# Performance work log

Measured on AMD Instinct MI355X. Metric: run time of the kernel, lower is better.

## Reference

```python
import jax, jax.numpy as jnp
import numpy as np

DENSITY_FACTOR = 100.0
RAY_SAMPLES = 256
W_RES, H_RES = 320, 240
BS = 4
VOL_D = 128


def setup_inputs() -> dict:
    key = jax.random.key(0)
    k1, k2 = jax.random.split(key)
    vol = jax.random.uniform(k1, (BS, 4, VOL_D, VOL_D, VOL_D), dtype=jnp.float32)
    # per-batch rigid rotation about the y axis (homogeneous 4x4, w component stays 1)
    ang = jax.random.uniform(k2, (BS,), minval=0.0, maxval=2.0 * np.pi, dtype=jnp.float32)
    c, s = jnp.cos(ang), jnp.sin(ang)
    z, o = jnp.zeros_like(c), jnp.ones_like(c)
    tfm = jnp.stack([
        jnp.stack([c, z, s, z], -1),
        jnp.stack([z, o, z, z], -1),
        jnp.stack([-s, z, c, z], -1),
        jnp.stack([z, z, z, o], -1),
    ], axis=1)  # (BS,4,4)
    return {"vol": vol, "tfm": tfm}


def grid_sample_3d(vol, grid):
    """torch.nn.functional.grid_sample (5D, trilinear, zeros padding, align_corners=False).
    vol: (C,D,H,W); grid: (S,Hh,Ww,3) with last dim = (x,y,z) in [-1,1]. -> (C,S,Hh,Ww)"""
    C, D, H, W = vol.shape
    gx, gy, gz = grid[..., 0], grid[..., 1], grid[..., 2]
    # unnormalize, align_corners=False convention
    ix = ((gx + 1.0) * W - 1.0) * 0.5
    iy = ((gy + 1.0) * H - 1.0) * 0.5
    iz = ((gz + 1.0) * D - 1.0) * 0.5
    ix0, iy0, iz0 = jnp.floor(ix), jnp.floor(iy), jnp.floor(iz)
    fx, fy, fz = ix - ix0, iy - iy0, iz - iz0
    out = jnp.zeros((C,) + grid.shape[:-1], vol.dtype)
    for dz in (0, 1):
        for dy in (0, 1):
            for dx in (0, 1):
                xi, yi, zi = ix0 + dx, iy0 + dy, iz0 + dz
                w = ((fx if dx else 1.0 - fx) * (fy if dy else 1.0 - fy)
                     * (fz if dz else 1.0 - fz))
                valid = ((xi >= 0) & (xi < W) & (yi >= 0) & (yi < H)
                         & (zi >= 0) & (zi < D))
                xc = jnp.clip(xi, 0, W - 1).astype(jnp.int32)
                yc = jnp.clip(yi, 0, H - 1).astype(jnp.int32)
                zc = jnp.clip(zi, 0, D - 1).astype(jnp.int32)
                v = vol[:, zc, yc, xc]  # (C,S,Hh,Ww) gather
                out = out + v * (w * valid.astype(vol.dtype))[None]
    return out


def _sample_coords(tfm):
    """Build the transformed sample grid: (BS, S, H, W, 3)."""
    z = jnp.linspace(-1.0, 1.0, RAY_SAMPLES)
    y = jnp.linspace(-1.0, 1.0, H_RES)
    x = jnp.linspace(-1.0, 1.0, W_RES)
    Z, Y, X = jnp.meshgrid(z, y, x, indexing='ij')  # torch.meshgrid default 'ij'
    coords = jnp.stack([X, Y, Z, jnp.ones_like(X)], axis=-1)  # (S,H,W,4) homogenized
    flat = coords.reshape(-1, 4)
    tc = jnp.einsum('bij,nj->bni', tfm, flat).reshape(
        tfm.shape[0], RAY_SAMPLES, H_RES, W_RES, 4)
    return tc[..., :3] / tc[..., 3:4]


def reference(vol, tfm):
    density = vol[:, 3:4]            # (B,1,D,H,W)
    color = vol[:, :3]               # (B,3,D,H,W)
    grid = _sample_coords(tfm.astype(vol.dtype))  # (B,S,H,W,3)
    dens = density * (DENSITY_FACTOR / RAY_SAMPLES)
    ds = jax.vmap(grid_sample_3d)(dens, grid)        # (B,1,S,H,W)
    transmission = jnp.cumprod(1.0 - ds, axis=2)     # sequential scan over rays
    weight = ds * transmission                       # (B,1,S,H,W)
    w_sum = jnp.sum(weight, axis=2)                  # (B,1,H,W)
    cs = jax.vmap(grid_sample_3d)(color, grid)       # (B,3,S,H,W)
    render = jnp.sum(weight * cs, axis=2) / (w_sum + 1e-6)  # (B,3,H,W)
    alpha = 1.0 - transmission[:, :, -1]             # == 1 - prod(1-ds, axis=2)
    return render * alpha
```

## Files before the change

kernel.cpp:

```cpp
#include <hip/hip_runtime.h>
#include <hip/hip_fp16.h>

namespace {

constexpr int W_RES = 320, H_RES = 240, BS = 4, VD = 128, NS = 256;
constexpr float DENS_SCALE = 100.0f / 256.0f;
constexpr float TAU = 5e-4f;
constexpr long long VOX = (long long)VD * VD * VD;

__device__ __forceinline__ unsigned h2u(__half2 h) {
    unsigned u; __builtin_memcpy(&u, &h, 4); return u;
}
__device__ __forceinline__ __half2 u2h(unsigned u) {
    __half2 h; __builtin_memcpy(&h, &u, 4); return h;
}

__global__ void transpose_k(const float* __restrict__ vol, uint4* __restrict__ out) {
    long long tid = (long long)blockIdx.x * blockDim.x + threadIdx.x;
    const long long npair = (long long)BS * VOX / 2;
    if (tid >= npair) return;
    int b = (int)(tid / (VOX / 2));
    long long r2 = (tid - (long long)b * (VOX / 2)) * 2;
    const float* vb = vol + (long long)b * 4 * VOX + r2;
    float2 R = *(const float2*)(vb);
    float2 G = *(const float2*)(vb + VOX);
    float2 Bc = *(const float2*)(vb + 2 * VOX);
    float2 Dn = *(const float2*)(vb + 3 * VOX);
    uint4 o;
    o.x = h2u(__floats2half2_rn(R.x, G.x));
    o.y = h2u(__floats2half2_rn(Bc.x, Dn.x));
    o.z = h2u(__floats2half2_rn(R.y, G.y));
    o.w = h2u(__floats2half2_rn(Bc.y, Dn.y));
    out[tid] = o;
}

struct Stage {
    uint2 p[8];
    float w[8];
};

struct Coord {
    int x0, y0, z0;
    float fx, fy, fz;
    bool fast;
};

__device__ __forceinline__ Coord make_coord(float ix, float iy, float iz) {
    Coord c;
    float fx0 = floorf(ix), fy0 = floorf(iy), fz0 = floorf(iz);
    c.fx = ix - fx0; c.fy = iy - fy0; c.fz = iz - fz0;
    c.x0 = (int)fx0; c.y0 = (int)fy0; c.z0 = (int)fz0;
    c.fast = ((unsigned)c.x0 < 127u) & ((unsigned)c.y0 < 127u) & ((unsigned)c.z0 < 127u);
    return c;
}

__device__ __forceinline__ void weights_plain(const Coord& c, Stage& st) {
    float wx0 = 1.0f - c.fx, wx1 = c.fx;
    float wy0 = 1.0f - c.fy, wy1 = c.fy;
    float wz0 = 1.0f - c.fz, wz1 = c.fz;
    float w00 = wz0 * wy0, w01 = wz0 * wy1, w10 = wz1 * wy0, w11 = wz1 * wy1;
    st.w[0] = w00 * wx0; st.w[1] = w00 * wx1;
    st.w[2] = w01 * wx0; st.w[3] = w01 * wx1;
    st.w[4] = w10 * wx0; st.w[5] = w10 * wx1;
    st.w[6] = w11 * wx0; st.w[7] = w11 * wx1;
}

__device__ __forceinline__ void stage_fast(const uint2* __restrict__ vb,
                                           const Coord& c, Stage& st) {
    const uint2* r0 = vb + ((c.z0 * VD + c.y0) * VD + c.x0);
    const uint2* r1 = r0 + VD * VD;
    st.p[0] = r0[0];      st.p[1] = r0[1];
    st.p[2] = r0[VD];     st.p[3] = r0[VD + 1];
    st.p[4] = r1[0];      st.p[5] = r1[1];
    st.p[6] = r1[VD];     st.p[7] = r1[VD + 1];
    weights_plain(c, st);
}

__device__ __forceinline__ void stage_safe(const uint2* __restrict__ vb,
                                           const Coord& c, Stage& st) {
    int x0 = c.x0, y0 = c.y0, z0 = c.z0;
    float mx0 = ((unsigned)x0 < 128u) ? 1.0f : 0.0f;
    float mx1 = ((unsigned)(x0 + 1) < 128u) ? 1.0f : 0.0f;
    float my0 = ((unsigned)y0 < 128u) ? 1.0f : 0.0f;
    float my1 = ((unsigned)(y0 + 1) < 128u) ? 1.0f : 0.0f;
    float mz0 = ((unsigned)z0 < 128u) ? 1.0f : 0.0f;
    float mz1 = ((unsigned)(z0 + 1) < 128u) ? 1.0f : 0.0f;
    float wx0 = (1.0f - c.fx) * mx0, wx1 = c.fx * mx1;
    float wy0 = (1.0f - c.fy) * my0, wy1 = c.fy * my1;
    float wz0 = (1.0f - c.fz) * mz0, wz1 = c.fz * mz1;

    int xc0 = min(max(x0, 0), 127), xc1 = min(max(x0 + 1, 0), 127);
    int yc0 = min(max(y0, 0), 127), yc1 = min(max(y0 + 1, 0), 127);
    int zc0 = min(max(z0, 0), 127), zc1 = min(max(z0 + 1, 0), 127);

    int r00 = (zc0 * VD + yc0) * VD, r01 = (zc0 * VD + yc1) * VD;
    int r10 = (zc1 * VD + yc0) * VD, r11 = (zc1 * VD + yc1) * VD;

    st.p[0] = vb[r00 + xc0]; st.p[1] = vb[r00 + xc1];
    st.p[2] = vb[r01 + xc0]; st.p[3] = vb[r01 + xc1];
    st.p[4] = vb[r10 + xc0]; st.p[5] = vb[r10 + xc1];
    st.p[6] = vb[r11 + xc0]; st.p[7] = vb[r11 + xc1];

    float w00 = wz0 * wy0, w01 = wz0 * wy1, w10 = wz1 * wy0, w11 = wz1 * wy1;
    st.w[0] = w00 * wx0; st.w[1] = w00 * wx1;
    st.w[2] = w01 * wx0; st.w[3] = w01 * wx1;
    st.w[4] = w10 * wx0; st.w[5] = w10 * wx1;
    st.w[6] = w11 * wx0; st.w[7] = w11 * wx1;
}

__device__ __forceinline__ void consume(const Stage& st, float& T, float& wsum,
                                        float& aR, float& aG, float& aB) {
    float ax0 = 0, ay0 = 0, az0 = 0, aw0 = 0;
    float ax1 = 0, ay1 = 0, az1 = 0, aw1 = 0;
#pragma unroll
    for (int i = 0; i < 8; i += 2) {
        __half2 rg0 = u2h(st.p[i].x), bd0 = u2h(st.p[i].y);
        __half2 rg1 = u2h(st.p[i + 1].x), bd1 = u2h(st.p[i + 1].y);
        ax0 = fmaf(st.w[i], __half2float(__low2half(rg0)), ax0);
        ay0 = fmaf(st.w[i], __half2float(__high2half(rg0)), ay0);
        az0 = fmaf(st.w[i], __half2float(__low2half(bd0)), az0);
        aw0 = fmaf(st.w[i], __half2float(__high2half(bd0)), aw0);
        ax1 = fmaf(st.w[i + 1], __half2float(__low2half(rg1)), ax1);
        ay1 = fmaf(st.w[i + 1], __half2float(__high2half(rg1)), ay1);
        az1 = fmaf(st.w[i + 1], __half2float(__low2half(bd1)), az1);
        aw1 = fmaf(st.w[i + 1], __half2float(__high2half(bd1)), aw1);
    }
    float dsv = (aw0 + aw1) * DENS_SCALE;
    T *= (1.0f - dsv);
    float wgt = dsv * T;
    wsum += wgt;
    aR = fmaf(wgt, ax0 + ax1, aR);
    aG = fmaf(wgt, ay0 + ay1, aG);
    aB = fmaf(wgt, az0 + az1, aB);
}

__global__ void __launch_bounds__(256) raycast_k(const uint2* __restrict__ vol8,
                                                 const float* __restrict__ tfm,
                                                 float* __restrict__ out) {
    constexpr int NPIX = W_RES * H_RES;
    int lane = threadIdx.x & 63;
    int wave = threadIdx.x >> 6;
    int bx = blockIdx.x % (W_RES / 16);
    int rest = blockIdx.x / (W_RES / 16);
    int by = rest % (H_RES / 16);
    int b = rest / (H_RES / 16);
    int x = bx * 16 + (lane & 15);
    int y = by * 16 + wave * 4 + (lane >> 4);

    float X = -1.0f + 2.0f * x / (float)(W_RES - 1);
    float Y = -1.0f + 2.0f * y / (float)(H_RES - 1);
    const float dZ = 2.0f / (float)(NS - 1);

    const float* M = tfm + b * 16;
    float bxc = M[0] * X + M[1] * Y + M[3];
    float byc = M[4] * X + M[5] * Y + M[7];
    float bzc = M[8] * X + M[9] * Y + M[11];
    float bwc = M[12] * X + M[13] * Y + M[15];
    float m02 = M[2], m12 = M[6], m22 = M[10], m32 = M[14];

    const uint2* vb = vol8 + (long long)b * VOX;

    bool w1 = (fabsf(bwc - 1.0f) < 1e-6f) && (fabsf(m32) < 1e-6f);
    float lo = 0.0f, hi = (float)(NS - 1);
    if (w1) {
        const float LIM = 1.0078125f + 1e-5f;
        auto clipAxis = [&](float bb, float mm) {
            float A = bb - mm;
            float B = mm * dZ;
            if (fabsf(B) < 1e-9f) {
                if (fabsf(A) > LIM) { lo = 1.0f; hi = 0.0f; }
            } else {
                float s1 = (-LIM - A) / B, s2 = (LIM - A) / B;
                lo = fmaxf(lo, fminf(s1, s2));
                hi = fminf(hi, fmaxf(s1, s2));
            }
        };
        clipAxis(bxc, m02);
        clipAxis(byc, m12);
        clipAxis(bzc, m22);
    }
    int s_start = max(0, (int)ceilf(lo - 1e-3f));
    int s_end = min(NS - 1, (int)floorf(hi + 1e-3f));

    int wsv = s_start, wev = s_end;
#pragma unroll
    for (int off = 1; off < 64; off <<= 1) {
        wsv = min(wsv, __shfl_xor(wsv, off));
        wev = max(wev, __shfl_xor(wev, off));
    }

    auto coords = [&](int s, float& ix, float& iy, float& iz) {
        float Z = fmaf((float)s, dZ, -1.0f);
        float gx = fmaf(m02, Z, bxc);
        float gy = fmaf(m12, Z, byc);
        float gz = fmaf(m22, Z, bzc);
        if (!w1) {
            float iw = 1.0f / fmaf(m32, Z, bwc);
            gx *= iw; gy *= iw; gz *= iw;
        }
        ix = fmaf(gx, 64.0f, 63.5f);
        iy = fmaf(gy, 64.0f, 63.5f);
        iz = fmaf(gz, 64.0f, 63.5f);
    };

    float T = 1.0f, wsum = 0.0f, aR = 0.0f, aG = 0.0f, aB = 0.0f;
    Stage A, B, C;

    for (int s = wsv; s <= wev; s += 3) {
        bool alive = (T >= TAU);
        bool g0 = (s >= s_start) & (s <= s_end) & alive;
        bool g1 = (s + 1 >= s_start) & (s + 1 <= s_end) & alive;
        bool g2 = (s + 2 >= s_start) & (s + 2 <= s_end) & alive;
        Coord c0, c1, c2;
        float ix, iy, iz;
        if (g0) { coords(s, ix, iy, iz); c0 = make_coord(ix, iy, iz); }
        if (g1) { coords(s + 1, ix, iy, iz); c1 = make_coord(ix, iy, iz); }
        if (g2) { coords(s + 2, ix, iy, iz); c2 = make_coord(ix, iy, iz); }
        bool fastAll = __all((g0 ? c0.fast : true) & (g1 ? c1.fast : true) &
                             (g2 ? c2.fast : true));
        if (fastAll) {
            if (g0) stage_fast(vb, c0, A);
            if (g1) stage_fast(vb, c1, B);
            if (g2) stage_fast(vb, c2, C);
        } else {
            if (g0) stage_safe(vb, c0, A);
            if (g1) stage_safe(vb, c1, B);
            if (g2) stage_safe(vb, c2, C);
        }
        __builtin_amdgcn_sched_barrier(0);
        if (g0) consume(A, T, wsum, aR, aG, aB);
        if (g1 & (T >= TAU)) consume(B, T, wsum, aR, aG, aB);
        if (g2 & (T >= TAU)) consume(C, T, wsum, aR, aG, aB);
        if (!__any((T >= TAU) & (s + 3 <= s_end))) break;
    }

    float scale = (1.0f - T) / (wsum + 1e-6f);
    int po = y * W_RES + x;
    float* ob = out + (long long)b * 3 * NPIX;
    ob[po] = aR * scale;
    ob[po + NPIX] = aG * scale;
    ob[po + 2 * NPIX] = aB * scale;
}

}

extern "C" void kernel_launch(void* const* d_in, const int* in_sizes, int n_in,
                              void* d_out, int out_size, void* d_ws, size_t ws_size,
                              hipStream_t stream) {
    const float* vol = (const float*)d_in[0];
    const float* tfm = (const float*)d_in[1];
    float* out = (float*)d_out;

    uint4* v16 = (uint4*)d_ws;
    (void)ws_size; (void)in_sizes; (void)n_in; (void)out_size;

    const long long npair = (long long)BS * VOX / 2;
    transpose_k<<<(int)((npair + 255) / 256), 256, 0, stream>>>(vol, v16);

    const int nblk = (W_RES / 16) * (H_RES / 16) * BS;
    raycast_k<<<nblk, 256, 0, stream>>>((const uint2*)v16, tfm, out);
}
```

Before: 173.0 us.

## Quantize volume to RGBA8, use persistent atomic tile scheduler with center-out ordering

Converts the packed volume from fp16 RGBA (8 bytes per voxel) to 8-bit unorm RGBA (4 bytes per voxel), halving gather bandwidth and cache footprint, and rescales density and color in the consumer. The raycast kernel becomes persistent: 2048 single-wave blocks pull 16x4 pixel tiles from an atomic counter, ordered center-out and interleaved across batches, to balance uneven ray lengths. The inner loop now steps by 4 samples without per-sample validity guards. The loss of guards and 8-bit quantization add accuracy risk, and the counter reset relies on the transpose kernel running first.

```diff
diff --git a/kernel.cpp b/kernel.cpp
--- a/kernel.cpp
+++ b/kernel.cpp
@@ -1,41 +1,44 @@
 #include <hip/hip_runtime.h>
-#include <hip/hip_fp16.h>
 
 namespace {
 
 constexpr int W_RES = 320, H_RES = 240, BS = 4, VD = 128, NS = 256;
-constexpr float DENS_SCALE = 100.0f / 256.0f;
+constexpr float DENS_SCALE = 100.0f / 256.0f / 255.0f;
 constexpr float TAU = 5e-4f;
 constexpr long long VOX = (long long)VD * VD * VD;
-
-__device__ __forceinline__ unsigned h2u(__half2 h) {
-    unsigned u; __builtin_memcpy(&u, &h, 4); return u;
-}
-__device__ __forceinline__ __half2 u2h(unsigned u) {
-    __half2 h; __builtin_memcpy(&h, &u, 4); return h;
-}
-
-__global__ void transpose_k(const float* __restrict__ vol, uint4* __restrict__ out) {
+constexpr int NTILE = (W_RES / 16) * (H_RES / 4) * BS;
+constexpr size_t CTR_OFF = (size_t)BS * VOX * 4;
+
+__global__ void transpose_k(const float* __restrict__ vol, uint4* __restrict__ out,
+                            unsigned* __restrict__ ctr) {
     long long tid = (long long)blockIdx.x * blockDim.x + threadIdx.x;
-    const long long npair = (long long)BS * VOX / 2;
-    if (tid >= npair) return;
-    int b = (int)(tid / (VOX / 2));
-    long long r2 = (tid - (long long)b * (VOX / 2)) * 2;
-    const float* vb = vol + (long long)b * 4 * VOX + r2;
-    float2 R = *(const float2*)(vb);
-    float2 G = *(const float2*)(vb + VOX);
-    float2 Bc = *(const float2*)(vb + 2 * VOX);
-    float2 Dn = *(const float2*)(vb + 3 * VOX);
+    if (tid == 0) *ctr = 0u;
+    const long long nq = (long long)BS * VOX / 4;
+    if (tid >= nq) return;
+    int b = (int)(tid / (VOX / 4));
+    long long r4 = (tid - (long long)b * (VOX / 4)) * 4;
+    const float* vb = vol + (long long)b * 4 * VOX + r4;
+    float4 R = *(const float4*)(vb);
+    float4 G = *(const float4*)(vb + VOX);
+    float4 Bc = *(const float4*)(vb + 2 * VOX);
+    float4 Dn = *(const float4*)(vb + 3 * VOX);
+    auto pk = [](float r, float g, float bl, float d) -> unsigned {
+        unsigned ur = (unsigned)(r * 255.0f + 0.5f);
+        unsigned ug = (unsigned)(g * 255.0f + 0.5f);
+        unsigned ub = (unsigned)(bl * 255.0f + 0.5f);
+        unsigned ud = (unsigned)(d * 255.0f + 0.5f);
+        return ur | (ug << 8) | (ub << 16) | (ud << 24);
+    };
     uint4 o;
-    o.x = h2u(__floats2half2_rn(R.x, G.x));
-    o.y = h2u(__floats2half2_rn(Bc.x, Dn.x));
-    o.z = h2u(__floats2half2_rn(R.y, G.y));
-    o.w = h2u(__floats2half2_rn(Bc.y, Dn.y));
+    o.x = pk(R.x, G.x, Bc.x, Dn.x);
+    o.y = pk(R.y, G.y, Bc.y, Dn.y);
+    o.z = pk(R.z, G.z, Bc.z, Dn.z);
+    o.w = pk(R.w, G.w, Bc.w, Dn.w);
     out[tid] = o;
 }
 
-struct Stage {
-    uint2 p[8];
+struct St {
+    unsigned p[8];
     float w[8];
 };
 
@@ -45,19 +48,21 @@
     bool fast;
 };
 
-__device__ __forceinline__ Coord make_coord(float ix, float iy, float iz) {
+__device__ __forceinline__ Coord mkc(float ix, float iy, float iz) {
     Coord c;
-    float fx0 = floorf(ix), fy0 = floorf(iy), fz0 = floorf(iz);
-    c.fx = ix - fx0; c.fy = iy - fy0; c.fz = iz - fz0;
-    c.x0 = (int)fx0; c.y0 = (int)fy0; c.z0 = (int)fz0;
+    float f;
+    f = floorf(ix); c.fx = ix - f; c.x0 = (int)f;
+    f = floorf(iy); c.fy = iy - f; c.y0 = (int)f;
+    f = floorf(iz); c.fz = iz - f; c.z0 = (int)f;
     c.fast = ((unsigned)c.x0 < 127u) & ((unsigned)c.y0 < 127u) & ((unsigned)c.z0 < 127u);
     return c;
 }
 
-__device__ __forceinline__ void weights_plain(const Coord& c, Stage& st) {
-    float wx0 = 1.0f - c.fx, wx1 = c.fx;
-    float wy0 = 1.0f - c.fy, wy1 = c.fy;
-    float wz0 = 1.0f - c.fz, wz1 = c.fz;
+__device__ __forceinline__ void wts(const Coord& c, St& st, float mx0, float mx1,
+                                    float my0, float my1, float mz0, float mz1) {
+    float wx0 = (1.0f - c.fx) * mx0, wx1 = c.fx * mx1;
+    float wy0 = (1.0f - c.fy) * my0, wy1 = c.fy * my1;
+    float wz0 = (1.0f - c.fz) * mz0, wz1 = c.fz * mz1;
     float w00 = wz0 * wy0, w01 = wz0 * wy1, w10 = wz1 * wy0, w11 = wz1 * wy1;
     st.w[0] = w00 * wx0; st.w[1] = w00 * wx1;
     st.w[2] = w01 * wx0; st.w[3] = w01 * wx1;
@@ -65,19 +70,19 @@
     st.w[6] = w11 * wx0; st.w[7] = w11 * wx1;
 }
 
-__device__ __forceinline__ void stage_fast(const uint2* __restrict__ vb,
-                                           const Coord& c, Stage& st) {
-    const uint2* r0 = vb + ((c.z0 * VD + c.y0) * VD + c.x0);
-    const uint2* r1 = r0 + VD * VD;
-    st.p[0] = r0[0];      st.p[1] = r0[1];
-    st.p[2] = r0[VD];     st.p[3] = r0[VD + 1];
-    st.p[4] = r1[0];      st.p[5] = r1[1];
-    st.p[6] = r1[VD];     st.p[7] = r1[VD + 1];
-    weights_plain(c, st);
-}
-
-__device__ __forceinline__ void stage_safe(const uint2* __restrict__ vb,
-                                           const Coord& c, Stage& st) {
+__device__ __forceinline__ void stage_fast(const unsigned* __restrict__ vb,
+                                           const Coord& c, St& st) {
+    const unsigned* r0 = vb + ((c.z0 * VD + c.y0) * VD + c.x0);
+    const unsigned* r1 = r0 + VD * VD;
+    st.p[0] = r0[0];  st.p[1] = r0[1];
+    st.p[2] = r0[VD]; st.p[3] = r0[VD + 1];
+    st.p[4] = r1[0];  st.p[5] = r1[1];
+    st.p[6] = r1[VD]; st.p[7] = r1[VD + 1];
+    wts(c, st, 1, 1, 1, 1, 1, 1);
+}
+
+__device__ __forceinline__ void stage_safe(const unsigned* __restrict__ vb,
+                                           const Coord& c, St& st) {
     int x0 = c.x0, y0 = c.y0, z0 = c.z0;
     float mx0 = ((unsigned)x0 < 128u) ? 1.0f : 0.0f;
     float mx1 = ((unsigned)(x0 + 1) < 128u) ? 1.0f : 0.0f;
@@ -85,9 +90,6 @@
     float my1 = ((unsigned)(y0 + 1) < 128u) ? 1.0f : 0.0f;
     float mz0 = ((unsigned)z0 < 128u) ? 1.0f : 0.0f;
     float mz1 = ((unsigned)(z0 + 1) < 128u) ? 1.0f : 0.0f;
-    float wx0 = (1.0f - c.fx) * mx0, wx1 = c.fx * mx1;
-    float wy0 = (1.0f - c.fy) * my0, wy1 = c.fy * my1;
-    float wz0 = (1.0f - c.fz) * mz0, wz1 = c.fz * mz1;
 
     int xc0 = min(max(x0, 0), 127), xc1 = min(max(x0 + 1, 0), 127);
     int yc0 = min(max(y0, 0), 127), yc1 = min(max(y0 + 1, 0), 127);
@@ -101,145 +103,144 @@
     st.p[4] = vb[r10 + xc0]; st.p[5] = vb[r10 + xc1];
     st.p[6] = vb[r11 + xc0]; st.p[7] = vb[r11 + xc1];
 
-    float w00 = wz0 * wy0, w01 = wz0 * wy1, w10 = wz1 * wy0, w11 = wz1 * wy1;
-    st.w[0] = w00 * wx0; st.w[1] = w00 * wx1;
-    st.w[2] = w01 * wx0; st.w[3] = w01 * wx1;
-    st.w[4] = w10 * wx0; st.w[5] = w10 * wx1;
-    st.w[6] = w11 * wx0; st.w[7] = w11 * wx1;
-}
-
-__device__ __forceinline__ void consume(const Stage& st, float& T, float& wsum,
+    wts(c, st, mx0, mx1, my0, my1, mz0, mz1);
+}
+
+__device__ __forceinline__ void consume(const St& st, float& T, float& wsum,
                                         float& aR, float& aG, float& aB) {
-    float ax0 = 0, ay0 = 0, az0 = 0, aw0 = 0;
-    float ax1 = 0, ay1 = 0, az1 = 0, aw1 = 0;
+    float ar = 0, ag = 0, ab = 0, ad = 0;
 #pragma unroll
-    for (int i = 0; i < 8; i += 2) {
-        __half2 rg0 = u2h(st.p[i].x), bd0 = u2h(st.p[i].y);
-        __half2 rg1 = u2h(st.p[i + 1].x), bd1 = u2h(st.p[i + 1].y);
-        ax0 = fmaf(st.w[i], __half2float(__low2half(rg0)), ax0);
-        ay0 = fmaf(st.w[i], __half2float(__high2half(rg0)), ay0);
-        az0 = fmaf(st.w[i], __half2float(__low2half(bd0)), az0);
-        aw0 = fmaf(st.w[i], __half2float(__high2half(bd0)), aw0);
-        ax1 = fmaf(st.w[i + 1], __half2float(__low2half(rg1)), ax1);
-        ay1 = fmaf(st.w[i + 1], __half2float(__high2half(rg1)), ay1);
-        az1 = fmaf(st.w[i + 1], __half2float(__low2half(bd1)), az1);
-        aw1 = fmaf(st.w[i + 1], __half2float(__high2half(bd1)), aw1);
+    for (int i = 0; i < 8; ++i) {
+        unsigned cv = st.p[i];
+        float w = st.w[i];
+        ar = fmaf(w, (float)(cv & 255u), ar);
+        ag = fmaf(w, (float)((cv >> 8) & 255u), ag);
+        ab = fmaf(w, (float)((cv >> 16) & 255u), ab);
+        ad = fmaf(w, (float)(cv >> 24), ad);
     }
-    float dsv = (aw0 + aw1) * DENS_SCALE;
+    float dsv = ad * DENS_SCALE;
     T *= (1.0f - dsv);
     float wgt = dsv * T;
     wsum += wgt;
-    aR = fmaf(wgt, ax0 + ax1, aR);
-    aG = fmaf(wgt, ay0 + ay1, aG);
-    aB = fmaf(wgt, az0 + az1, aB);
-}
-
-__global__ void __launch_bounds__(256) raycast_k(const uint2* __restrict__ vol8,
-                                                 const float* __restrict__ tfm,
-                                                 float* __restrict__ out) {
+    aR = fmaf(wgt, ar, aR);
+    aG = fmaf(wgt, ag, aG);
+    aB = fmaf(wgt, ab, aB);
+}
+
+__global__ void __launch_bounds__(64) raycast_k(const unsigned* __restrict__ vol,
+                                                const float* __restrict__ tfm,
+                                                float* __restrict__ out,
+                                                unsigned* __restrict__ ctr) {
     constexpr int NPIX = W_RES * H_RES;
-    int lane = threadIdx.x & 63;
-    int wave = threadIdx.x >> 6;
-    int bx = blockIdx.x % (W_RES / 16);
-    int rest = blockIdx.x / (W_RES / 16);
-    int by = rest % (H_RES / 16);
-    int b = rest / (H_RES / 16);
-    int x = bx * 16 + (lane & 15);
-    int y = by * 16 + wave * 4 + (lane >> 4);
-
-    float X = -1.0f + 2.0f * x / (float)(W_RES - 1);
-    float Y = -1.0f + 2.0f * y / (float)(H_RES - 1);
+    const int lane = threadIdx.x;
     const float dZ = 2.0f / (float)(NS - 1);
 
-    const float* M = tfm + b * 16;
-    float bxc = M[0] * X + M[1] * Y + M[3];
-    float byc = M[4] * X + M[5] * Y + M[7];
-    float bzc = M[8] * X + M[9] * Y + M[11];
-    float bwc = M[12] * X + M[13] * Y + M[15];
-    float m02 = M[2], m12 = M[6], m22 = M[10], m32 = M[14];
-
-    const uint2* vb = vol8 + (long long)b * VOX;
-
-    bool w1 = (fabsf(bwc - 1.0f) < 1e-6f) && (fabsf(m32) < 1e-6f);
-    float lo = 0.0f, hi = (float)(NS - 1);
-    if (w1) {
-        const float LIM = 1.0078125f + 1e-5f;
-        auto clipAxis = [&](float bb, float mm) {
-            float A = bb - mm;
-            float B = mm * dZ;
-            if (fabsf(B) < 1e-9f) {
-                if (fabsf(A) > LIM) { lo = 1.0f; hi = 0.0f; }
+    while (true) {
+        unsigned n = 0;
+        if (lane == 0) n = atomicAdd(ctr, 1u);
+        n = (unsigned)__shfl((int)n, 0);
+        if (n >= (unsigned)NTILE) return;
+
+        int b = n & 3;
+        int k = n >> 2;
+        int cxr = k / 60;
+        int ryr = k - cxr * 60;
+        int tx = (cxr & 1) ? (9 - (cxr >> 1)) : (10 + (cxr >> 1));
+        int ty = (ryr & 1) ? (29 - (ryr >> 1)) : (30 + (ryr >> 1));
+        int x = tx * 16 + (lane & 15);
+        int y = ty * 4 + (lane >> 4);
+
+        float X = -1.0f + 2.0f * x / (float)(W_RES - 1);
+        float Y = -1.0f + 2.0f * y / (float)(H_RES - 1);
+
+        const float* M = tfm + b * 16;
+        float bxc = M[0] * X + M[1] * Y + M[3];
+        float byc = M[4] * X + M[5] * Y + M[7];
+        float bzc = M[8] * X + M[9] * Y + M[11];
+        float bwc = M[12] * X + M[13] * Y + M[15];
+        float m02 = M[2], m12 = M[6], m22 = M[10], m32 = M[14];
+
+        const unsigned* vb = vol + (long long)b * VOX;
+
+        bool w1 = (fabsf(bwc - 1.0f) < 1e-6f) && (fabsf(m32) < 1e-6f);
+        float lo = 0.0f, hi = (float)(NS - 1);
+        if (w1) {
+            const float LIM = 1.0078125f + 1e-5f;
+            auto clipAxis = [&](float bb, float mm) {
+                float A = bb - mm;
+                float Bq = mm * dZ;
+                if (fabsf(Bq) < 1e-9f) {
+                    if (fabsf(A) > LIM) { lo = 1.0f; hi = 0.0f; }
+                } else {
+                    float s1 = (-LIM - A) / Bq, s2 = (LIM - A) / Bq;
+                    lo = fmaxf(lo, fminf(s1, s2));
+                    hi = fminf(hi, fmaxf(s1, s2));
+                }
+            };
+            clipAxis(bxc, m02);
+            clipAxis(byc, m12);
+            clipAxis(bzc, m22);
+        }
+        int s_start = max(0, (int)ceilf(lo - 1e-3f));
+        int s_end = min(NS - 1, (int)floorf(hi + 1e-3f));
+
+        int wsv = s_start, wev = s_end;
+#pragma unroll
+        for (int off = 1; off < 64; off <<= 1) {
+            wsv = min(wsv, __shfl_xor(wsv, off));
+            wev = max(wev, __shfl_xor(wev, off));
+        }
+
+        auto coords = [&](int s, float& ix, float& iy, float& iz) {
+            float Z = fmaf((float)s, dZ, -1.0f);
+            float gx = fmaf(m02, Z, bxc);
+            float gy = fmaf(m12, Z, byc);
+            float gz = fmaf(m22, Z, bzc);
+            if (!w1) {
+                float iw = 1.0f / fmaf(m32, Z, bwc);
+                gx *= iw; gy *= iw; gz *= iw;
+            }
+            ix = fmaf(gx, 64.0f, 63.5f);
+            iy = fmaf(gy, 64.0f, 63.5f);
+            iz = fmaf(gz, 64.0f, 63.5f);
+        };
+
+        float T = 1.0f, wsum = 0.0f, aR = 0.0f, aG = 0.0f, aB = 0.0f;
+        St S0, S1, S2, S3;
+
+        for (int s = wsv; s <= wev; s += 4) {
+            float ix, iy, iz;
+            coords(s, ix, iy, iz);      Coord c0 = mkc(ix, iy, iz);
+            coords(s + 1, ix, iy, iz);  Coord c1 = mkc(ix, iy, iz);
+            coords(s + 2, ix, iy, iz);  Coord c2 = mkc(ix, iy, iz);
+            coords(s + 3, ix, iy, iz);  Coord c3 = mkc(ix, iy, iz);
+            bool fast = __all(c0.fast & c1.fast & c2.fast & c3.fast);
+            if (fast) {
+                stage_fast(vb, c0, S0);
+                stage_fast(vb, c1, S1);
+                stage_fast(vb, c2, S2);
+                stage_fast(vb, c3, S3);
             } else {
-                float s1 = (-LIM - A) / B, s2 = (LIM - A) / B;
-                lo = fmaxf(lo, fminf(s1, s2));
-                hi = fminf(hi, fmaxf(s1, s2));
+                stage_safe(vb, c0, S0);
+                stage_safe(vb, c1, S1);
+                stage_safe(vb, c2, S2);
+                stage_safe(vb, c3, S3);
             }
-        };
-        clipAxis(bxc, m02);
-        clipAxis(byc, m12);
-        clipAxis(bzc, m22);
+            __builtin_amdgcn_sched_barrier(0);
+            consume(S0, T, wsum, aR, aG, aB);
+            consume(S1, T, wsum, aR, aG, aB);
+            consume(S2, T, wsum, aR, aG, aB);
+            consume(S3, T, wsum, aR, aG, aB);
+            if (!__any(T >= TAU)) break;
+        }
+
+        float scale = (1.0f - T) / (wsum + 1e-6f) * (1.0f / 255.0f);
+        int po = y * W_RES + x;
+        float* ob = out + (long long)b * 3 * NPIX;
+        ob[po] = aR * scale;
+        ob[po + NPIX] = aG * scale;
+        ob[po + 2 * NPIX] = aB * scale;
     }
-    int s_start = max(0, (int)ceilf(lo - 1e-3f));
-    int s_end = min(NS - 1, (int)floorf(hi + 1e-3f));
-
-    int wsv = s_start, wev = s_end;
-#pragma unroll
-    for (int off = 1; off < 64; off <<= 1) {
-        wsv = min(wsv, __shfl_xor(wsv, off));
-        wev = max(wev, __shfl_xor(wev, off));
-    }
-
-    auto coords = [&](int s, float& ix, float& iy, float& iz) {
-        float Z = fmaf((float)s, dZ, -1.0f);
-        float gx = fmaf(m02, Z, bxc);
-        float gy = fmaf(m12, Z, byc);
-        float gz = fmaf(m22, Z, bzc);
-        if (!w1) {
-            float iw = 1.0f / fmaf(m32, Z, bwc);
-            gx *= iw; gy *= iw; gz *= iw;
-        }
-        ix = fmaf(gx, 64.0f, 63.5f);
-        iy = fmaf(gy, 64.0f, 63.5f);
-        iz = fmaf(gz, 64.0f, 63.5f);
-    };
-
-    float T = 1.0f, wsum = 0.0f, aR = 0.0f, aG = 0.0f, aB = 0.0f;
-    Stage A, B, C;
-
-    for (int s = wsv; s <= wev; s += 3) {
-        bool alive = (T >= TAU);
-        bool g0 = (s >= s_start) & (s <= s_end) & alive;
-        bool g1 = (s + 1 >= s_start) & (s + 1 <= s_end) & alive;
-        bool g2 = (s + 2 >= s_start) & (s + 2 <= s_end) & alive;
-        Coord c0, c1, c2;
-        float ix, iy, iz;
-        if (g0) { coords(s, ix, iy, iz); c0 = make_coord(ix, iy, iz); }
-        if (g1) { coords(s + 1, ix, iy, iz); c1 = make_coord(ix, iy, iz); }
-        if (g2) { coords(s + 2, ix, iy, iz); c2 = make_coord(ix, iy, iz); }
-        bool fastAll = __all((g0 ? c0.fast : true) & (g1 ? c1.fast : true) &
-                             (g2 ? c2.fast : true));
-        if (fastAll) {
-            if (g0) stage_fast(vb, c0, A);
-            if (g1) stage_fast(vb, c1, B);
-            if (g2) stage_fast(vb, c2, C);
-        } else {
-            if (g0) stage_safe(vb, c0, A);
-            if (g1) stage_safe(vb, c1, B);
-            if (g2) stage_safe(vb, c2, C);
-        }
-        __builtin_amdgcn_sched_barrier(0);
-        if (g0) consume(A, T, wsum, aR, aG, aB);
-        if (g1 & (T >= TAU)) consume(B, T, wsum, aR, aG, aB);
-        if (g2 & (T >= TAU)) consume(C, T, wsum, aR, aG, aB);
-        if (!__any((T >= TAU) & (s + 3 <= s_end))) break;
-    }
-
-    float scale = (1.0f - T) / (wsum + 1e-6f);
-    int po = y * W_RES + x;
-    float* ob = out + (long long)b * 3 * NPIX;
-    ob[po] = aR * scale;
-    ob[po + NPIX] = aG * scale;
-    ob[po + 2 * NPIX] = aB * scale;
 }
 
 }
@@ -251,12 +252,13 @@
     const float* tfm = (const float*)d_in[1];
     float* out = (float*)d_out;
 
-    uint4* v16 = (uint4*)d_ws;
+    unsigned char* ws = (unsigned char*)d_ws;
+    uint4* v8 = (uint4*)ws;
+    unsigned* ctr = (unsigned*)(ws + CTR_OFF);
     (void)ws_size; (void)in_sizes; (void)n_in; (void)out_size;
 
-    const long long npair = (long long)BS * VOX / 2;
-    transpose_k<<<(int)((npair + 255) / 256), 256, 0, stream>>>(vol, v16);
-
-    const int nblk = (W_RES / 16) * (H_RES / 16) * BS;
-    raycast_k<<<nblk, 256, 0, stream>>>((const uint2*)v16, tfm, out);
-}
+    const long long nq = (long long)BS * VOX / 4;
+    transpose_k<<<(int)((nq + 255) / 256), 256, 0, stream>>>(vol, v8, ctr);
+
+    raycast_k<<<2048, 64, 0, stream>>>((const unsigned*)v8, tfm, out, ctr);
+}
```

Result: slower. 201.5 us (+16.5%).
